# Kernel optimization log

Hardware: AMD Instinct MI355X
Metric: run time of the kernel (lower is better)

The kernel has to match this reference:

```python
import jax, jax.numpy as jnp
import numpy as np

R, N = 4096, 128          # rays, samples per ray
POSE_L, DIR_L = 10, 4     # NeRF frequency counts


def posenc(x, L):
    # x: [..., 3] -> [..., 3 + 3*2*L]
    freqs = (2.0 ** jnp.arange(L, dtype=x.dtype))  # [L]
    xf = x[..., None, :] * freqs[:, None]          # [..., L, 3]
    enc = jnp.concatenate([jnp.sin(xf), jnp.cos(xf)], axis=-1)  # [..., L, 6]
    enc = enc.reshape(x.shape[:-1] + (-1,))
    return jnp.concatenate([x, enc], axis=-1)


def setup_inputs() -> dict:
    key = jax.random.key(0)
    ks = jax.random.split(key, 16)
    def w(k, shape, fan_in):
        return (jax.random.normal(k, shape, jnp.float32) / np.sqrt(fan_in)).astype(jnp.float32)
    ray = jax.random.normal(ks[0], (R, 6), jnp.float32)
    t = jax.random.uniform(ks[1], (R, N + 1, 1), jnp.float32) * 4.0  # unsorted depths
    return {
        "ray": ray, "t": t,
        "W0": w(ks[2], (63, 256), 63),   "b0": jnp.zeros((256,), jnp.float32),
        "W1": w(ks[3], (256, 256), 256), "b1": jnp.zeros((256,), jnp.float32),
        "W2": w(ks[4], (256, 256), 256), "b2": jnp.zeros((256,), jnp.float32),
        "Ws": w(ks[5], (256, 1), 256),   "bs": jnp.zeros((1,), jnp.float32),
        "Wc1": w(ks[6], (283, 128), 283), "bc1": jnp.zeros((128,), jnp.float32),
        "Wc2": w(ks[7], (128, 3), 128),  "bc2": jnp.zeros((3,), jnp.float32),
    }


def _nerf_render(ray, t, W0, b0, W1, b1, W2, b2, Ws, bs, Wc1, bc1, Wc2, bc2):
    o = ray[:, None, :3]                       # [R,1,3]
    d = ray[:, None, 3:]                       # [R,1,3]
    x = o + t[:, 1:, :] * d                    # [R,N,3]
    xe = posenc(x, POSE_L)                     # [R,N,63]
    de = jnp.broadcast_to(posenc(d, DIR_L), (x.shape[0], x.shape[1], 27))  # [R,N,27]

    h = jax.nn.relu(xe @ W0 + b0)
    h = jax.nn.relu(h @ W1 + b1)
    h = jax.nn.relu(h @ W2 + b2)               # [R,N,256]
    sigma = jax.nn.softplus(h @ Ws + bs)       # [R,N,1]
    hc = jax.nn.relu(jnp.concatenate([h, de], axis=-1) @ Wc1 + bc1)
    color = jax.nn.sigmoid(hc @ Wc2 + bc2)     # [R,N,3]

    # integrate(): alpha compositing along the sample dim
    ts = jnp.sort(t, axis=-2)                  # [R,N+1,1]
    dt = ts[:, 1:, :] - ts[:, :-1, :]          # [R,N,1]
    sdt = sigma * dt                           # [R,N,1]
    Ti = jnp.exp(-jnp.cumsum(sdt, axis=-2))[:, :-1, :]          # [R,N-1,1]
    Ti = jnp.concatenate([jnp.ones_like(Ti[:, :1, :]), Ti], axis=-2)  # [R,N,1]
    alpha = 1.0 - jnp.exp(-sdt)
    wi = Ti * alpha                            # [R,N,1]
    rgb = (wi * color).sum(axis=-2)            # [R,3]
    return rgb, wi


def reference(ray, t, W0, b0, W1, b1, W2, b2, Ws, bs, Wc1, bc1, Wc2, bc2):
    return _nerf_render(ray, t, W0, b0, W1, b1, W2, b2, Ws, bs, Wc1, bc1, Wc2, bc2)
```

## Files before the change

kernel.cpp:

```cpp
#include <hip/hip_runtime.h>
#include <hip/hip_bf16.h>
#include <math.h>

constexpr int R_ = 4096;

typedef __attribute__((ext_vector_type(8))) short short8;
typedef __attribute__((ext_vector_type(4))) float f32x4;
typedef __attribute__((ext_vector_type(16))) float f32x16;
typedef __attribute__((ext_vector_type(2))) unsigned int uint2v;

#define MFMA32(a, b, c) __builtin_amdgcn_mfma_f32_32x32x16_bf16(a, b, c, 0, 0, 0)

union U4 { unsigned int u[4]; short8 s8; };

__device__ __forceinline__ unsigned short f2bf(float f) {
    unsigned int u = __float_as_uint(f);
    u += 0x7fffu + ((u >> 16) & 1u);
    return (unsigned short)(u >> 16);
}

__device__ __forceinline__ unsigned int cvtpk(float lo, float hi) {
    unsigned int d;
    asm("v_cvt_pk_bf16_f32 %0, %1, %2" : "=v"(d) : "v"(lo), "v"(hi));
    return d;
}
__device__ __forceinline__ void swap32(unsigned int& a, unsigned int& b) {
    uint2v r = __builtin_amdgcn_permlane32_swap(a, b, false, false);
    a = r[0]; b = r[1];
}

__device__ __forceinline__ short8 pack_half(float a0, float a1, float a2, float a3,
                                            float b0, float b1, float b2, float b3) {
    unsigned int x0 = cvtpk(a0, a1), x1 = cvtpk(a2, a3);
    unsigned int x2 = cvtpk(b0, b1), x3 = cvtpk(b2, b3);
    swap32(x0, x2);
    swap32(x1, x3);
    U4 t; t.u[0] = x0; t.u[1] = x1; t.u[2] = x2; t.u[3] = x3;
    return t.s8;
}

__global__ __launch_bounds__(256) void prep_weights(
    const float* __restrict__ W0, const float* __restrict__ W1,
    const float* __restrict__ W2, const float* __restrict__ Wc1,
    unsigned short* __restrict__ out)
{
    int i = blockIdx.x * 256 + threadIdx.x;
    if (i >= 180224) return;
    float val;
    if (i < 16384) {
        int j = i & 7, l = (i >> 3) & 63, q = i >> 9;
        int ks = q & 3, ct = q >> 2, ls = l & 31, hi = l >> 5;
        int n = ct * 32 + ls, k = ks * 16 + hi * 8 + j;
        val = (k < 63) ? W0[k * 256 + n] : 0.f;
    } else if (i < 81920) {
        int e = i - 16384;
        int j = e & 7, l = (e >> 3) & 63, q = e >> 9;
        int ks = q & 15, ct = q >> 4, ls = l & 31, hi = l >> 5;
        int n = ct * 32 + ls, k = ks * 16 + hi * 8 + j;
        val = W1[k * 256 + n];
    } else if (i < 147456) {
        int e = i - 81920;
        int j = e & 7, l = (e >> 3) & 63, q = e >> 9;
        int ks = q & 15, ct = q >> 4, ls = l & 31, hi = l >> 5;
        int n = ct * 32 + ls, k = ks * 16 + hi * 8 + j;
        val = W2[k * 256 + n];
    } else {
        int e = i - 147456;
        int j = e & 7, l = (e >> 3) & 63, q = e >> 9;
        int ks = q & 15, ct = q >> 4, ls = l & 31, hi = l >> 5;
        int n = ct * 32 + ls, k = ks * 16 + hi * 8 + j;
        val = Wc1[k * 128 + n];
    }
    out[i] = f2bf(val);
}

template <bool DO_SIGMA, bool DO_PACK, bool DO_COLOR>
__device__ __forceinline__ void epilog(
    const f32x16& acc, int ct,
    const float* __restrict__ wsv, const float* __restrict__ wc2R,
    int hi, short8* __restrict__ Bout,
    float& sp, float& c0, float& c1, float& c2)
{
    float rr[16];
    #pragma unroll
    for (int i = 0; i < 16; ++i) rr[i] = fmaxf(acc[i], 0.f);
    if constexpr (DO_SIGMA) {
        #pragma unroll
        for (int g = 0; g < 4; ++g) {
            f32x4 wv = *(const f32x4*)&wsv[ct * 32 + 4 * hi + 8 * g];
            sp = fmaf(rr[4*g+0], wv[0], sp);
            sp = fmaf(rr[4*g+1], wv[1], sp);
            sp = fmaf(rr[4*g+2], wv[2], sp);
            sp = fmaf(rr[4*g+3], wv[3], sp);
        }
    }
    if constexpr (DO_COLOR) {
        #pragma unroll
        for (int g = 0; g < 4; ++g) {
            int nb = ct * 32 + 4 * hi + 8 * g;
            f32x4 w0 = *(const f32x4*)&wc2R[0 * 128 + nb];
            f32x4 w1 = *(const f32x4*)&wc2R[1 * 128 + nb];
            f32x4 w2 = *(const f32x4*)&wc2R[2 * 128 + nb];
            #pragma unroll
            for (int i = 0; i < 4; ++i) {
                c0 = fmaf(rr[4*g+i], w0[i], c0);
                c1 = fmaf(rr[4*g+i], w1[i], c1);
                c2 = fmaf(rr[4*g+i], w2[i], c2);
            }
        }
    }
    if constexpr (DO_PACK) {
        Bout[2*ct+0] = pack_half(rr[0], rr[1], rr[2],  rr[3],
                                 rr[4], rr[5], rr[6],  rr[7]);
        Bout[2*ct+1] = pack_half(rr[8], rr[9], rr[10], rr[11],
                                 rr[12], rr[13], rr[14], rr[15]);
    }
}

template <int NT, bool DO_SIGMA, bool DO_PACK, bool DO_COLOR>
__device__ __forceinline__ void mlp_layer(
    const unsigned short* __restrict__ wbase,
    const float* __restrict__ biasv,
    const float* __restrict__ wsv,
    const float* __restrict__ wc2R,
    int lane, int hi,
    const short8 (&Bin)[16], short8* __restrict__ Bout,
    float& sp, float& c0, float& c1, float& c2)
{
    const short8* __restrict__ w = (const short8*)wbase + lane;
    short8 A[4], B4[4];
    #pragma unroll
    for (int j = 0; j < 4; ++j) A[j] = w[j * 64];
    #pragma unroll
    for (int ct = 0; ct < NT; ++ct) {
        f32x16 acc;
        #pragma unroll
        for (int g = 0; g < 4; ++g) {
            f32x4 bv = *(const f32x4*)&biasv[ct * 32 + 4 * hi + 8 * g];
            acc[4*g+0]=bv[0]; acc[4*g+1]=bv[1]; acc[4*g+2]=bv[2]; acc[4*g+3]=bv[3];
        }
        #pragma unroll
        for (int j = 0; j < 4; ++j) B4[j] = w[(ct * 16 + 4 + j) * 64];
        #pragma unroll
        for (int j = 0; j < 4; ++j) acc = MFMA32(A[j], Bin[j], acc);
        #pragma unroll
        for (int j = 0; j < 4; ++j) A[j] = w[(ct * 16 + 8 + j) * 64];
        #pragma unroll
        for (int j = 0; j < 4; ++j) acc = MFMA32(B4[j], Bin[4 + j], acc);
        #pragma unroll
        for (int j = 0; j < 4; ++j) B4[j] = w[(ct * 16 + 12 + j) * 64];
        #pragma unroll
        for (int j = 0; j < 4; ++j) acc = MFMA32(A[j], Bin[8 + j], acc);
        if (ct + 1 < NT) {
            #pragma unroll
            for (int j = 0; j < 4; ++j) A[j] = w[((ct + 1) * 16 + j) * 64];
        }
        #pragma unroll
        for (int j = 0; j < 4; ++j) acc = MFMA32(B4[j], Bin[12 + j], acc);
        epilog<DO_SIGMA, DO_PACK, DO_COLOR>(acc, ct, wsv, wc2R, hi, Bout,
                                            sp, c0, c1, c2);
        __syncthreads();
    }
}

__global__ __launch_bounds__(256, 2) void nerf_kernel(
    const float* __restrict__ ray, const float* __restrict__ t,
    const float* __restrict__ b0g, const float* __restrict__ b1g,
    const float* __restrict__ b2g,
    const float* __restrict__ Wsg, const float* __restrict__ bsg,
    const float* __restrict__ Wc1g, const float* __restrict__ bc1g,
    const float* __restrict__ Wc2g, const float* __restrict__ bc2g,
    const unsigned short* __restrict__ wt,
    float* __restrict__ rgb_out, float* __restrict__ wi_out)
{
    __shared__ __align__(16) unsigned char s_xe[128 * 128];
    __shared__ __align__(16) float s_bias[896];
    __shared__ __align__(16) float s_ws[256];
    __shared__ __align__(16) float s_wc2R[384];
    __shared__ float s_sigma[128];
    __shared__ float s_color[384];
    __shared__ float s_de[27];
    __shared__ float s_od[6];
    __shared__ float s_t[129];
    __shared__ float s_ts[129];
    __shared__ float s_sdt[128];
    __shared__ float s_cum[128];
    __shared__ float s_wi[128];

    const int tid  = threadIdx.x;
    const int wv   = tid >> 6;
    const int lane = tid & 63;
    const int r    = blockIdx.x;
    const int ls   = lane & 31;
    const int hi   = lane >> 5;
    const int row  = wv * 32 + ls;
    const int sw   = (ls & 7) << 4;

    if (tid < 6) s_od[tid] = ray[r * 6 + tid];
    __syncthreads();
    const float d0 = s_od[3], d1 = s_od[4], d2 = s_od[5];

    s_bias[tid] = b0g[tid];
    s_bias[256 + tid] = b1g[tid];
    s_bias[512 + tid] = b2g[tid];
    s_ws[tid] = Wsg[tid];
    for (int i = tid; i < 384; i += 256) {
        int c = i >> 7, n = i & 127;
        s_wc2R[i] = Wc2g[n * 3 + c];
    }
    if (tid < 129) s_t[tid] = t[r * 129 + tid];
    if (tid < 27) {
        int f = tid; float v;
        if (f < 3) v = (f == 0) ? d0 : ((f == 1) ? d1 : d2);
        else {
            int q = f - 3, l = q / 6, rm = q % 6, c = rm % 3;
            float dc = (c == 0) ? d0 : ((c == 1) ? d1 : d2);
            float a = dc * (float)(1 << l);
            v = (rm < 3) ? sinf(a) : cosf(a);
        }
        s_de[f] = v;
    }
    __syncthreads();

    {
        const int p = tid & 127;
        const int psw = (p & 7) << 4;
        unsigned char* xp = s_xe + p * 128;
        float tv = t[r * 129 + 1 + p];
        if (tid < 128) {
            #pragma unroll
            for (int cgi = 0; cgi < 2; ++cgi) {
                float x = s_od[cgi] + tv * s_od[cgi + 3];
                *(unsigned short*)(xp + ((2 * cgi) ^ psw)) = f2bf(x);
                float sv = sinf(x), cv = cosf(x);
                #pragma unroll
                for (int l = 0; l < 10; ++l) {
                    *(unsigned short*)(xp + ((2 * (3 + 6 * l + cgi)) ^ psw)) = f2bf(sv);
                    *(unsigned short*)(xp + ((2 * (6 + 6 * l + cgi)) ^ psw)) = f2bf(cv);
                    float ns = 2.f * sv * cv, nc = 1.f - 2.f * sv * sv;
                    sv = ns; cv = nc;
                }
            }
        } else {
            float x = s_od[2] + tv * s_od[5];
            *(unsigned short*)(xp + (4 ^ psw)) = f2bf(x);
            float sv = sinf(x), cv = cosf(x);
            #pragma unroll
            for (int l = 0; l < 10; ++l) {
                *(unsigned short*)(xp + ((2 * (5 + 6 * l)) ^ psw)) = f2bf(sv);
                *(unsigned short*)(xp + ((2 * (8 + 6 * l)) ^ psw)) = f2bf(cv);
                float ns = 2.f * sv * cv, nc = 1.f - 2.f * sv * sv;
                sv = ns; cv = nc;
            }
            *(unsigned short*)(xp + (126 ^ psw)) = 0;
            float acc = bc1g[p];
            for (int k = 0; k < 27; ++k)
                acc = fmaf(s_de[k], Wc1g[(256 + k) * 128 + p], acc);
            s_bias[768 + p] = acc;
        }
    }
    __syncthreads();

    short8 BA[16], BB[16];
    float sp = 0.f, c0 = 0.f, c1 = 0.f, c2 = 0.f;

    {
        short8 BX[4];
        #pragma unroll
        for (int ks = 0; ks < 4; ++ks)
            BX[ks] = *(const short8*)(s_xe + row * 128 + ((32 * ks + 16 * hi) ^ sw));
        const short8* __restrict__ w0 = (const short8*)wt + lane;
        short8 Q0[4], Q1[4];
        #pragma unroll
        for (int j = 0; j < 4; ++j) Q0[j] = w0[j * 64];
        #pragma unroll
        for (int ct = 0; ct < 8; ++ct) {
            if (ct + 1 < 8) {
                #pragma unroll
                for (int j = 0; j < 4; ++j)
                    Q1[j] = w0[((ct + 1) * 4 + j) * 64];
            }
            f32x16 acc;
            #pragma unroll
            for (int g = 0; g < 4; ++g) {
                f32x4 bv = *(const f32x4*)&s_bias[ct * 32 + 4 * hi + 8 * g];
                acc[4*g+0]=bv[0]; acc[4*g+1]=bv[1]; acc[4*g+2]=bv[2]; acc[4*g+3]=bv[3];
            }
            #pragma unroll
            for (int j = 0; j < 4; ++j) acc = MFMA32(Q0[j], BX[j], acc);
            epilog<false, true, false>(acc, ct, nullptr, nullptr, hi, BA,
                                       sp, c0, c1, c2);
            #pragma unroll
            for (int j = 0; j < 4; ++j) Q0[j] = Q1[j];
        }
    }

    mlp_layer<8, false, true, false>(wt + 16384, s_bias + 256, nullptr, nullptr,
                                     lane, hi, BA, BB, sp, c0, c1, c2);
    mlp_layer<8, true, true, false>(wt + 81920, s_bias + 512, s_ws, nullptr,
                                    lane, hi, BB, BA, sp, c0, c1, c2);
    sp += __shfl_xor(sp, 32);
    if (lane < 32) {
        float x = sp + bsg[0];
        s_sigma[row] = fmaxf(x, 0.f) + log1pf(expf(-fabsf(x)));
    }
    mlp_layer<4, false, false, true>(wt + 147456, s_bias + 768, nullptr, s_wc2R,
                                     lane, hi, BA, BB, sp, c0, c1, c2);
    c0 += __shfl_xor(c0, 32);
    c1 += __shfl_xor(c1, 32);
    c2 += __shfl_xor(c2, 32);
    if (lane < 32) {
        s_color[row * 3 + 0] = 1.f / (1.f + expf(-(c0 + bc2g[0])));
        s_color[row * 3 + 1] = 1.f / (1.f + expf(-(c1 + bc2g[1])));
        s_color[row * 3 + 2] = 1.f / (1.f + expf(-(c2 + bc2g[2])));
    }
    __syncthreads();

    if (tid < 129) {
        float v = s_t[tid];
        int rank = 0;
        for (int j = 0; j < 129; ++j) {
            float u = s_t[j];
            rank += (u < v) || (u == v && j < tid);
        }
        s_ts[rank] = v;
    }
    __syncthreads();
    if (tid < 128) {
        float dt = s_ts[tid + 1] - s_ts[tid];
        float sd = s_sigma[tid] * dt;
        s_sdt[tid] = sd;
        s_cum[tid] = sd;
    }
    __syncthreads();
    for (int off = 1; off < 128; off <<= 1) {
        float add = (tid < 128 && tid >= off) ? s_cum[tid - off] : 0.f;
        __syncthreads();
        if (tid < 128) s_cum[tid] += add;
        __syncthreads();
    }
    if (tid < 128) {
        float Ti = (tid == 0) ? 1.f : expf(-s_cum[tid - 1]);
        float alpha = 1.f - expf(-s_sdt[tid]);
        float w = Ti * alpha;
        s_wi[tid] = w;
        wi_out[r * 128 + tid] = w;
    }
    __syncthreads();
    if (tid < 3) {
        float acc = 0.f;
        for (int i = 0; i < 128; ++i)
            acc = fmaf(s_wi[i], s_color[i * 3 + tid], acc);
        rgb_out[r * 3 + tid] = acc;
    }
}

extern "C" void kernel_launch(void* const* d_in, const int* in_sizes, int n_in,
                              void* d_out, int out_size, void* d_ws, size_t ws_size,
                              hipStream_t stream)
{
    const float* ray = (const float*)d_in[0];
    const float* t   = (const float*)d_in[1];
    const float* W0  = (const float*)d_in[2];
    const float* b0  = (const float*)d_in[3];
    const float* W1  = (const float*)d_in[4];
    const float* b1  = (const float*)d_in[5];
    const float* W2  = (const float*)d_in[6];
    const float* b2  = (const float*)d_in[7];
    const float* Ws  = (const float*)d_in[8];
    const float* bs  = (const float*)d_in[9];
    const float* Wc1 = (const float*)d_in[10];
    const float* bc1 = (const float*)d_in[11];
    const float* Wc2 = (const float*)d_in[12];
    const float* bc2 = (const float*)d_in[13];

    unsigned short* wt = (unsigned short*)d_ws;
    float* rgb_out = (float*)d_out;
    float* wi_out  = rgb_out + R_ * 3;

    hipLaunchKernelGGL(prep_weights, dim3(704), dim3(256), 0, stream,
                       W0, W1, W2, Wc1, wt);
    hipLaunchKernelGGL(nerf_kernel, dim3(R_), dim3(256), 0, stream,
                       ray, t, b0, b1, b2, Ws, bs, Wc1, bc1, Wc2, bc2,
                       wt, rgb_out, wi_out);
}
```

Measured before the change: 217.0 us.

## Process two rays per 512-thread block sharing weight setup

```diff
diff --git a/kernel.cpp b/kernel.cpp
--- a/kernel.cpp
+++ b/kernel.cpp
@@ -163,7 +163,7 @@
     }
 }
 
-__global__ __launch_bounds__(256, 2) void nerf_kernel(
+__global__ __launch_bounds__(512, 2) void nerf_kernel(
     const float* __restrict__ ray, const float* __restrict__ t,
     const float* __restrict__ b0g, const float* __restrict__ b1g,
     const float* __restrict__ b2g,
@@ -173,44 +173,48 @@
     const unsigned short* __restrict__ wt,
     float* __restrict__ rgb_out, float* __restrict__ wi_out)
 {
-    __shared__ __align__(16) unsigned char s_xe[128 * 128];
-    __shared__ __align__(16) float s_bias[896];
+    __shared__ __align__(16) unsigned char s_xe[2][128 * 128];
+    __shared__ __align__(16) float s_bias[768];
+    __shared__ __align__(16) float s_decont[2][128];
     __shared__ __align__(16) float s_ws[256];
     __shared__ __align__(16) float s_wc2R[384];
-    __shared__ float s_sigma[128];
-    __shared__ float s_color[384];
-    __shared__ float s_de[27];
-    __shared__ float s_od[6];
-    __shared__ float s_t[129];
-    __shared__ float s_ts[129];
-    __shared__ float s_sdt[128];
-    __shared__ float s_cum[128];
-    __shared__ float s_wi[128];
+    __shared__ float s_sigma[2][128];
+    __shared__ float s_color[2][384];
+    __shared__ float s_de[2][27];
+    __shared__ float s_od[2][6];
+    __shared__ float s_t[2][129];
+    __shared__ float s_ts[2][129];
+    __shared__ float s_sdt[2][128];
+    __shared__ float s_cum[2][128];
+    __shared__ float s_wi[2][128];
 
     const int tid  = threadIdx.x;
+    const int rh   = tid >> 8;
+    const int t2   = tid & 255;
     const int wv   = tid >> 6;
     const int lane = tid & 63;
-    const int r    = blockIdx.x;
     const int ls   = lane & 31;
     const int hi   = lane >> 5;
-    const int row  = wv * 32 + ls;
+    const int lw   = wv & 3;
+    const int row  = lw * 32 + ls;
     const int sw   = (ls & 7) << 4;
-
-    if (tid < 6) s_od[tid] = ray[r * 6 + tid];
-    __syncthreads();
-    const float d0 = s_od[3], d1 = s_od[4], d2 = s_od[5];
-
-    s_bias[tid] = b0g[tid];
-    s_bias[256 + tid] = b1g[tid];
-    s_bias[512 + tid] = b2g[tid];
-    s_ws[tid] = Wsg[tid];
-    for (int i = tid; i < 384; i += 256) {
-        int c = i >> 7, n = i & 127;
-        s_wc2R[i] = Wc2g[n * 3 + c];
-    }
-    if (tid < 129) s_t[tid] = t[r * 129 + tid];
-    if (tid < 27) {
-        int f = tid; float v;
+    const int r    = blockIdx.x * 2 + rh;
+
+    if (tid < 12) s_od[tid / 6][tid % 6] = ray[(blockIdx.x * 2 + tid / 6) * 6 + tid % 6];
+    __syncthreads();
+    const float d0 = s_od[rh][3], d1 = s_od[rh][4], d2 = s_od[rh][5];
+
+    s_bias[tid < 256 ? tid : tid] = 0.f;
+    s_bias[tid] = (tid < 256) ? b0g[tid] : b1g[tid - 256];
+    if (tid < 256) s_bias[512 + tid] = b2g[tid];
+    if (tid < 256) s_ws[tid] = Wsg[tid];
+    if (tid < 384) {
+        int c = tid >> 7, n = tid & 127;
+        s_wc2R[tid] = Wc2g[n * 3 + c];
+    }
+    if (t2 < 129) s_t[rh][t2] = t[r * 129 + t2];
+    if (t2 < 27) {
+        int f = t2; float v;
         if (f < 3) v = (f == 0) ? d0 : ((f == 1) ? d1 : d2);
         else {
             int q = f - 3, l = q / 6, rm = q % 6, c = rm % 3;
@@ -218,19 +222,19 @@
             float a = dc * (float)(1 << l);
             v = (rm < 3) ? sinf(a) : cosf(a);
         }
-        s_de[f] = v;
+        s_de[rh][f] = v;
     }
     __syncthreads();
 
     {
-        const int p = tid & 127;
+        const int p = t2 & 127;
         const int psw = (p & 7) << 4;
-        unsigned char* xp = s_xe + p * 128;
+        unsigned char* xp = s_xe[rh] + p * 128;
         float tv = t[r * 129 + 1 + p];
-        if (tid < 128) {
+        if (t2 < 128) {
             #pragma unroll
             for (int cgi = 0; cgi < 2; ++cgi) {
-                float x = s_od[cgi] + tv * s_od[cgi + 3];
+                float x = s_od[rh][cgi] + tv * s_od[rh][cgi + 3];
                 *(unsigned short*)(xp + ((2 * cgi) ^ psw)) = f2bf(x);
                 float sv = sinf(x), cv = cosf(x);
                 #pragma unroll
@@ -242,7 +246,7 @@
                 }
             }
         } else {
-            float x = s_od[2] + tv * s_od[5];
+            float x = s_od[rh][2] + tv * s_od[rh][5];
             *(unsigned short*)(xp + (4 ^ psw)) = f2bf(x);
             float sv = sinf(x), cv = cosf(x);
             #pragma unroll
@@ -255,8 +259,8 @@
             *(unsigned short*)(xp + (126 ^ psw)) = 0;
             float acc = bc1g[p];
             for (int k = 0; k < 27; ++k)
-                acc = fmaf(s_de[k], Wc1g[(256 + k) * 128 + p], acc);
-            s_bias[768 + p] = acc;
+                acc = fmaf(s_de[rh][k], Wc1g[(256 + k) * 128 + p], acc);
+            s_decont[rh][p] = acc;
         }
     }
     __syncthreads();
@@ -268,7 +272,7 @@
         short8 BX[4];
         #pragma unroll
         for (int ks = 0; ks < 4; ++ks)
-            BX[ks] = *(const short8*)(s_xe + row * 128 + ((32 * ks + 16 * hi) ^ sw));
+            BX[ks] = *(const short8*)(s_xe[rh] + row * 128 + ((32 * ks + 16 * hi) ^ sw));
         const short8* __restrict__ w0 = (const short8*)wt + lane;
         short8 Q0[4], Q1[4];
         #pragma unroll
@@ -302,56 +306,56 @@
     sp += __shfl_xor(sp, 32);
     if (lane < 32) {
         float x = sp + bsg[0];
-        s_sigma[row] = fmaxf(x, 0.f) + log1pf(expf(-fabsf(x)));
-    }
-    mlp_layer<4, false, false, true>(wt + 147456, s_bias + 768, nullptr, s_wc2R,
+        s_sigma[rh][row] = fmaxf(x, 0.f) + log1pf(expf(-fabsf(x)));
+    }
+    mlp_layer<4, false, false, true>(wt + 147456, s_decont[rh], nullptr, s_wc2R,
                                      lane, hi, BA, BB, sp, c0, c1, c2);
     c0 += __shfl_xor(c0, 32);
     c1 += __shfl_xor(c1, 32);
     c2 += __shfl_xor(c2, 32);
     if (lane < 32) {
-        s_color[row * 3 + 0] = 1.f / (1.f + expf(-(c0 + bc2g[0])));
-        s_color[row * 3 + 1] = 1.f / (1.f + expf(-(c1 + bc2g[1])));
-        s_color[row * 3 + 2] = 1.f / (1.f + expf(-(c2 + bc2g[2])));
-    }
-    __syncthreads();
-
-    if (tid < 129) {
-        float v = s_t[tid];
+        s_color[rh][row * 3 + 0] = 1.f / (1.f + expf(-(c0 + bc2g[0])));
+        s_color[rh][row * 3 + 1] = 1.f / (1.f + expf(-(c1 + bc2g[1])));
+        s_color[rh][row * 3 + 2] = 1.f / (1.f + expf(-(c2 + bc2g[2])));
+    }
+    __syncthreads();
+
+    if (t2 < 129) {
+        float v = s_t[rh][t2];
         int rank = 0;
         for (int j = 0; j < 129; ++j) {
-            float u = s_t[j];
-            rank += (u < v) || (u == v && j < tid);
-        }
-        s_ts[rank] = v;
-    }
-    __syncthreads();
-    if (tid < 128) {
-        float dt = s_ts[tid + 1] - s_ts[tid];
-        float sd = s_sigma[tid] * dt;
-        s_sdt[tid] = sd;
-        s_cum[tid] = sd;
+            float u = s_t[rh][j];
+            rank += (u < v) || (u == v && j < t2);
+        }
+        s_ts[rh][rank] = v;
+    }
+    __syncthreads();
+    if (t2 < 128) {
+        float dt = s_ts[rh][t2 + 1] - s_ts[rh][t2];
+        float sd = s_sigma[rh][t2] * dt;
+        s_sdt[rh][t2] = sd;
+        s_cum[rh][t2] = sd;
     }
     __syncthreads();
     for (int off = 1; off < 128; off <<= 1) {
-        float add = (tid < 128 && tid >= off) ? s_cum[tid - off] : 0.f;
+        float add = (t2 < 128 && t2 >= off) ? s_cum[rh][t2 - off] : 0.f;
         __syncthreads();
-        if (tid < 128) s_cum[tid] += add;
+        if (t2 < 128) s_cum[rh][t2] += add;
         __syncthreads();
     }
-    if (tid < 128) {
-        float Ti = (tid == 0) ? 1.f : expf(-s_cum[tid - 1]);
-        float alpha = 1.f - expf(-s_sdt[tid]);
+    if (t2 < 128) {
+        float Ti = (t2 == 0) ? 1.f : expf(-s_cum[rh][t2 - 1]);
+        float alpha = 1.f - expf(-s_sdt[rh][t2]);
         float w = Ti * alpha;
-        s_wi[tid] = w;
-        wi_out[r * 128 + tid] = w;
-    }
-    __syncthreads();
-    if (tid < 3) {
+        s_wi[rh][t2] = w;
+        wi_out[r * 128 + t2] = w;
+    }
+    __syncthreads();
+    if (t2 < 3) {
         float acc = 0.f;
         for (int i = 0; i < 128; ++i)
-            acc = fmaf(s_wi[i], s_color[i * 3 + tid], acc);
-        rgb_out[r * 3 + tid] = acc;
+            acc = fmaf(s_wi[rh][i], s_color[rh][i * 3 + t2], acc);
+        rgb_out[r * 3 + t2] = acc;
     }
 }
 
@@ -380,7 +384,7 @@
 
     hipLaunchKernelGGL(prep_weights, dim3(704), dim3(256), 0, stream,
                        W0, W1, W2, Wc1, wt);
-    hipLaunchKernelGGL(nerf_kernel, dim3(R_), dim3(256), 0, stream,
+    hipLaunchKernelGGL(nerf_kernel, dim3(R_ / 2), dim3(512), 0, stream,
                        ray, t, b0, b1, b2, Ws, bs, Wc1, bc1, Wc2, bc2,
                        wt, rgb_out, wi_out);
 }
```

Measured after the change: 266.8 us. 1.23x slower.
